# Kernel tuning notes

Hardware: AMD Instinct MI355X
Metric: run time of the kernel (lower is better)

## Reference

```python
import jax, jax.numpy as jnp
import numpy as np

N, E = 50000, 800000
IN_DIM, HID, OUT = 128, 64, 64
NEG_SLOPE = 0.2  # PyG GATConv default leaky_relu slope


def glorot(key, shape):
    fan_in, fan_out = shape[0], shape[-1]
    lim = jnp.sqrt(6.0 / (fan_in + fan_out))
    return jax.random.uniform(key, shape, minval=-lim, maxval=lim, dtype=jnp.float32)


def setup_inputs() -> dict:
    key = jax.random.key(0)
    ks = jax.random.split(key, 10)
    x = jax.random.normal(ks[0], (N, IN_DIM), dtype=jnp.float32)
    edge_index = jax.random.randint(ks[1], (2, E), 0, N, dtype=jnp.int64)
    # GATConv layer 1: heads=2, concat=False
    W1 = glorot(ks[2], (IN_DIM, 2 * HID))
    att_src1 = glorot(ks[3], (1, 2, HID))[0]   # [2, HID]
    att_dst1 = glorot(ks[4], (1, 2, HID))[0]
    b1 = jnp.zeros((HID,), jnp.float32)
    # GATConv layer 2: heads=1, concat=False
    W2 = glorot(ks[5], (HID, OUT))
    att_src2 = glorot(ks[6], (1, 1, OUT))[0]   # [1, OUT]
    att_dst2 = glorot(ks[7], (1, 1, OUT))[0]
    b2 = jnp.zeros((OUT,), jnp.float32)
    return {"x": x, "edge_index": edge_index, "W1": W1, "att_src1": att_src1,
            "att_dst1": att_dst1, "b1": b1, "W2": W2, "att_src2": att_src2,
            "att_dst2": att_dst2, "b2": b2}


def gat_conv(x, src, dst, W, att_src, att_dst, bias, heads, out_ch):
    n = x.shape[0]
    h = (x @ W).reshape(n, heads, out_ch)              # [N,H,C]
    a_src = jnp.einsum('nhc,hc->nh', h, att_src)       # [N,H]
    a_dst = jnp.einsum('nhc,hc->nh', h, att_dst)
    e = jax.nn.leaky_relu(a_src[src] + a_dst[dst], NEG_SLOPE)  # [E,H]
    # softmax over incoming edges per destination node (stable)
    e_max = jax.ops.segment_max(e, dst, num_segments=n)
    ex = jnp.exp(e - e_max[dst])
    denom = jax.ops.segment_sum(ex, dst, num_segments=n)
    alpha = ex / (denom[dst] + 1e-16)                  # [E,H]
    msg = h[src] * alpha[:, :, None]                   # [E,H,C]
    out = jax.ops.segment_sum(msg, dst, num_segments=n)
    return out.mean(axis=1) + bias                     # concat=False -> head mean


def reference(x, edge_index, W1, att_src1, att_dst1, b1, W2, att_src2, att_dst2, b2):
    n = x.shape[0]
    loop = jnp.arange(n, dtype=edge_index.dtype)
    src = jnp.concatenate([edge_index[0], loop])       # PyG add_self_loops
    dst = jnp.concatenate([edge_index[1], loop])
    x1 = gat_conv(x, src, dst, W1, att_src1, att_dst1, b1, 2, HID)
    x1 = jax.nn.elu(x1)
    # eval mode: dropedge and dropout are identity
    out = gat_conv(x1, src, dst, W2, att_src2, att_dst2, b2, 1, OUT)
    return out
```

## Files before the change

### kernel.cpp

```cpp
#include <hip/hip_runtime.h>
#include <math.h>

#define IN_DIM 128
#define HID 64
#define CAP 64
#define NEG_SLOPE 0.2f

__device__ __forceinline__ float wmax(float v){
  #pragma unroll
  for (int o = 32; o > 0; o >>= 1) v = fmaxf(v, __shfl_xor(v, o));
  return v;
}
__device__ __forceinline__ float wsum(float v){
  #pragma unroll
  for (int o = 32; o > 0; o >>= 1) v += __shfl_xor(v, o);
  return v;
}

__device__ __forceinline__ unsigned short f2bf(float f){
  union { float f; unsigned u; } v; v.f = f;
  unsigned r = v.u + 0x7fffu + ((v.u >> 16) & 1u);
  return (unsigned short)(r >> 16);
}
__device__ __forceinline__ float bl(unsigned u){
  union { unsigned u; float f; } v; v.u = u << 16; return v.f;
}
__device__ __forceinline__ float bh(unsigned u){
  union { unsigned u; float f; } v; v.u = u & 0xffff0000u; return v.f;
}

__global__ void build_buckets(const int* __restrict__ ei, int E,
                              int* __restrict__ cnt, int* __restrict__ bucket){
  int e = blockIdx.x * 256 + threadIdx.x;
  if (e >= E) return;
  int s = ei[e];
  int d = ei[E + e];
  int p = atomicAdd(&cnt[d], 1);
  if (p < CAP) bucket[d * CAP + p] = s;
}

template<int K, int NC, int HEADS>
__global__ __launch_bounds__(256) void gemm_mfma(const float* __restrict__ X,
    const float* __restrict__ Wm, const float* __restrict__ asrc,
    const float* __restrict__ adst, unsigned short* __restrict__ Hb,
    float* __restrict__ aa, int n_rows)
{
  typedef __attribute__((ext_vector_type(8))) short bf16x8;
  typedef __attribute__((ext_vector_type(4))) float f32x4;
  constexpr int KP = K + 8;
  constexpr int CP = NC + 4;
  constexpr unsigned SM1 = (unsigned)(64 + NC) * KP * 2;
  constexpr unsigned SM2 = (unsigned)64 * CP * 4;
  __shared__ char smem[SM1 > SM2 ? SM1 : SM2];
  unsigned short* xa = (unsigned short*)smem;
  unsigned short* wt = xa + 64 * KP;
  int tid = threadIdx.x;
  int n0 = blockIdx.x * 64;

  for (int idx = tid; idx < 64 * (K / 4); idx += 256){
    int n  = idx / (K / 4);
    int k4 = idx % (K / 4);
    float4 v = make_float4(0.f, 0.f, 0.f, 0.f);
    if (n0 + n < n_rows) v = *(const float4*)&X[(size_t)(n0 + n) * K + k4 * 4];
    ushort4 pk; pk.x = f2bf(v.x); pk.y = f2bf(v.y); pk.z = f2bf(v.z); pk.w = f2bf(v.w);
    *(ushort4*)&xa[n * KP + k4 * 4] = pk;
  }
  for (int idx = tid; idx < (K / 2) * (NC / 4); idx += 256){
    int kp = idx / (NC / 4);
    int n4 = idx % (NC / 4);
    float4 wa = *(const float4*)&Wm[(size_t)(2 * kp) * NC + n4 * 4];
    float4 wb = *(const float4*)&Wm[(size_t)(2 * kp + 1) * NC + n4 * 4];
    const float* pa = &wa.x; const float* pb = &wb.x;
    #pragma unroll
    for (int u = 0; u < 4; u++){
      unsigned val = (unsigned)f2bf(pa[u]) | ((unsigned)f2bf(pb[u]) << 16);
      *(unsigned*)&wt[(n4 * 4 + u) * KP + 2 * kp] = val;
    }
  }
  __syncthreads();

  int lane = tid & 63, w = tid >> 6;
  int m = lane & 15, q = lane >> 4;
  constexpr int NF = NC / 64;
  int n_base = w * (NC / 4);
  f32x4 acc[4][NF];
  #pragma unroll
  for (int i = 0; i < 4; i++)
    #pragma unroll
    for (int j = 0; j < NF; j++)
      #pragma unroll
      for (int r = 0; r < 4; r++) acc[i][j][r] = 0.f;

  #pragma unroll
  for (int ks = 0; ks < K / 32; ks++){
    bf16x8 af[4], bg[NF];
    #pragma unroll
    for (int m4 = 0; m4 < 4; m4++)
      af[m4] = *(const bf16x8*)&xa[(m4 * 16 + m) * KP + ks * 32 + q * 8];
    #pragma unroll
    for (int nf = 0; nf < NF; nf++)
      bg[nf] = *(const bf16x8*)&wt[(n_base + nf * 16 + m) * KP + ks * 32 + q * 8];
    #pragma unroll
    for (int m4 = 0; m4 < 4; m4++)
      #pragma unroll
      for (int nf = 0; nf < NF; nf++)
        acc[m4][nf] = __builtin_amdgcn_mfma_f32_16x16x32_bf16(af[m4], bg[nf], acc[m4][nf], 0, 0, 0);
  }
  __syncthreads();
  float* C = (float*)smem;
  #pragma unroll
  for (int m4 = 0; m4 < 4; m4++)
    #pragma unroll
    for (int nf = 0; nf < NF; nf++)
      #pragma unroll
      for (int r = 0; r < 4; r++)
        C[(m4 * 16 + q * 4 + r) * CP + n_base + nf * 16 + m] = acc[m4][nf][r];
  __syncthreads();

  constexpr int CH = NC / 4;
  int row = tid >> 2;
  int c0 = (tid & 3) * CH;
  int n = n0 + row;
  int head = (HEADS == 2) ? (c0 >> 6) : 0;
  float s_p = 0.f, d_p = 0.f;
  unsigned short hb[CH];
  #pragma unroll
  for (int c = 0; c < CH; c += 4){
    f32x4 v = *(const f32x4*)&C[row * CP + c0 + c];
    #pragma unroll
    for (int u = 0; u < 4; u++){
      int ch = (c0 + c + u) & 63;
      s_p += v[u] * asrc[head * 64 + ch];
      d_p += v[u] * adst[head * 64 + ch];
      hb[c + u] = f2bf(v[u]);
    }
  }
  if (n < n_rows){
    #pragma unroll
    for (int c = 0; c < CH; c += 8){
      uint4 pk;
      pk.x = (unsigned)hb[c]     | ((unsigned)hb[c + 1] << 16);
      pk.y = (unsigned)hb[c + 2] | ((unsigned)hb[c + 3] << 16);
      pk.z = (unsigned)hb[c + 4] | ((unsigned)hb[c + 5] << 16);
      pk.w = (unsigned)hb[c + 6] | ((unsigned)hb[c + 7] << 16);
      *(uint4*)&Hb[(size_t)n * NC + c0 + c] = pk;
    }
  }
  s_p += __shfl_xor(s_p, 1);
  d_p += __shfl_xor(d_p, 1);
  if (HEADS == 2){
    if ((tid & 1) == 0 && n < n_rows){
      aa[(size_t)n * 4 + head]     = s_p;
      aa[(size_t)n * 4 + 2 + head] = d_p;
    }
  } else {
    s_p += __shfl_xor(s_p, 2);
    d_p += __shfl_xor(d_p, 2);
    if ((tid & 3) == 0 && n < n_rows){
      aa[(size_t)n * 2]     = s_p;
      aa[(size_t)n * 2 + 1] = d_p;
    }
  }
}

__global__ void agg_layer1(const int* __restrict__ cnt, const int* __restrict__ bucket,
                           const float* __restrict__ aa, const unsigned short* __restrict__ h1b,
                           const float* __restrict__ b1, float* __restrict__ x1, int n_nodes){
  int d = (blockIdx.x * blockDim.x + threadIdx.x) >> 6;
  int lane = threadIdx.x & 63;
  if (d >= n_nodes) return;
  int deg = cnt[d]; deg = deg < CAP ? deg : CAP;
  float2 adv = *(const float2*)&aa[d * 4 + 2];
  int s = -1;
  if (lane < deg) s = bucket[d * CAP + lane];
  else if (lane == deg) s = d;
  float e0 = -INFINITY, e1 = -INFINITY;
  if (s >= 0){
    float2 asv = *(const float2*)&aa[s * 4];
    float t0 = asv.x + adv.x;
    float t1 = asv.y + adv.y;
    e0 = t0 >= 0.f ? t0 : NEG_SLOPE * t0;
    e1 = t1 >= 0.f ? t1 : NEG_SLOPE * t1;
  }
  float m0 = wmax(e0), m1 = wmax(e1);
  float p0 = (s >= 0) ? __expf(e0 - m0) : 0.f;
  float p1 = (s >= 0) ? __expf(e1 - m1) : 0.f;
  float al0 = p0 / (wsum(p0) + 1e-16f);
  float al1 = p1 / (wsum(p1) + 1e-16f);
  int ne = deg + 1;
  int g = lane >> 4, c = lane & 15;
  float acc[8] = {0.f,0.f,0.f,0.f,0.f,0.f,0.f,0.f};
  #pragma unroll 4
  for (int j0 = 0; j0 < ne; j0 += 4){
    int j = j0 + g;
    int jj = j < ne ? j : 0;
    int sj = __shfl(s, jj);
    float a0 = __shfl(al0, jj);
    float a1 = __shfl(al1, jj);
    if (j >= ne){ a0 = 0.f; a1 = 0.f; }
    uint4 v = ((const uint4*)(h1b + (size_t)sj * 128))[c];
    float a = (c < 8) ? a0 : a1;
    acc[0] += a * bl(v.x); acc[1] += a * bh(v.x);
    acc[2] += a * bl(v.y); acc[3] += a * bh(v.y);
    acc[4] += a * bl(v.z); acc[5] += a * bh(v.z);
    acc[6] += a * bl(v.w); acc[7] += a * bh(v.w);
  }
  #pragma unroll
  for (int i = 0; i < 8; i++){
    acc[i] += __shfl_xor(acc[i], 16);
    acc[i] += __shfl_xor(acc[i], 32);
  }
  float outv[8];
  #pragma unroll
  for (int i = 0; i < 8; i++){
    float o = __shfl_xor(acc[i], 8);
    outv[i] = 0.5f * (acc[i] + o);
  }
  if (g == 0 && c < 8){
    float r[8];
    #pragma unroll
    for (int i = 0; i < 8; i++){
      float v = outv[i] + b1[c * 8 + i];
      r[i] = v > 0.f ? v : expm1f(v);
    }
    float* p = &x1[(size_t)d * 64 + c * 8];
    *(float4*)p       = make_float4(r[0], r[1], r[2], r[3]);
    *(float4*)(p + 4) = make_float4(r[4], r[5], r[6], r[7]);
  }
}

__global__ void agg_layer2(const int* __restrict__ cnt, const int* __restrict__ bucket,
                           const float* __restrict__ aa, const unsigned short* __restrict__ h2b,
                           const float* __restrict__ b2, float* __restrict__ out, int n_nodes){
  int d = (blockIdx.x * blockDim.x + threadIdx.x) >> 6;
  int lane = threadIdx.x & 63;
  if (d >= n_nodes) return;
  int deg = cnt[d]; deg = deg < CAP ? deg : CAP;
  float ad = aa[d * 2 + 1];
  int s = -1;
  if (lane < deg) s = bucket[d * CAP + lane];
  else if (lane == deg) s = d;
  float e = -INFINITY;
  if (s >= 0){
    float t = aa[s * 2 + 0] + ad;
    e = t >= 0.f ? t : NEG_SLOPE * t;
  }
  float m = wmax(e);
  float p = (s >= 0) ? __expf(e - m) : 0.f;
  float al = p / (wsum(p) + 1e-16f);
  int ne = deg + 1;
  int g = lane >> 3, c = lane & 7;
  float acc[8] = {0.f,0.f,0.f,0.f,0.f,0.f,0.f,0.f};
  #pragma unroll 4
  for (int j0 = 0; j0 < ne; j0 += 8){
    int j = j0 + g;
    int jj = j < ne ? j : 0;
    int sj = __shfl(s, jj);
    float a = __shfl(al, jj);
    if (j >= ne) a = 0.f;
    uint4 v = ((const uint4*)(h2b + (size_t)sj * 64))[c];
    acc[0] += a * bl(v.x); acc[1] += a * bh(v.x);
    acc[2] += a * bl(v.y); acc[3] += a * bh(v.y);
    acc[4] += a * bl(v.z); acc[5] += a * bh(v.z);
    acc[6] += a * bl(v.w); acc[7] += a * bh(v.w);
  }
  #pragma unroll
  for (int i = 0; i < 8; i++){
    acc[i] += __shfl_xor(acc[i], 8);
    acc[i] += __shfl_xor(acc[i], 16);
    acc[i] += __shfl_xor(acc[i], 32);
  }
  if (lane < 8){
    float r[8];
    #pragma unroll
    for (int i = 0; i < 8; i++) r[i] = acc[i] + b2[lane * 8 + i];
    float* q = &out[(size_t)d * 64 + lane * 8];
    *(float4*)q       = make_float4(r[0], r[1], r[2], r[3]);
    *(float4*)(q + 4) = make_float4(r[4], r[5], r[6], r[7]);
  }
}

extern "C" void kernel_launch(void* const* d_in, const int* in_sizes, int n_in,
                              void* d_out, int out_size, void* d_ws, size_t ws_size,
                              hipStream_t stream){
  const float* x     = (const float*)d_in[0];
  const int*   ei    = (const int*)d_in[1];
  const float* W1    = (const float*)d_in[2];
  const float* asrc1 = (const float*)d_in[3];
  const float* adst1 = (const float*)d_in[4];
  const float* b1    = (const float*)d_in[5];
  const float* W2    = (const float*)d_in[6];
  const float* asrc2 = (const float*)d_in[7];
  const float* adst2 = (const float*)d_in[8];
  const float* b2    = (const float*)d_in[9];
  float* out = (float*)d_out;
  int N = in_sizes[0] / IN_DIM;
  int E = in_sizes[1] / 2;

  char* p = (char*)d_ws;
  unsigned short* h1b = (unsigned short*)p;  p += (size_t)N * 128 * 2;
  unsigned short* h2b = (unsigned short*)p;  p += (size_t)N * 64 * 2;
  float* x1  = (float*)p;                    p += (size_t)N * 64 * 4;
  float* aa1 = (float*)p;                    p += (size_t)N * 4 * 4;
  float* aa2 = (float*)p;                    p += (size_t)N * 2 * 4;
  int* cnt    = (int*)p;                     p += (size_t)N * 4;
  int* bucket = (int*)p;

  hipMemsetAsync(cnt, 0, N * sizeof(int), stream);
  build_buckets<<<(E + 255) / 256, 256, 0, stream>>>(ei, E, cnt, bucket);
  gemm_mfma<128, 128, 2><<<(N + 63) / 64, 256, 0, stream>>>(
      x, W1, asrc1, adst1, h1b, aa1, N);
  agg_layer1<<<(N + 3) / 4, 256, 0, stream>>>(cnt, bucket, aa1, h1b, b1, x1, N);
  gemm_mfma<64, 64, 1><<<(N + 63) / 64, 256, 0, stream>>>(
      x1, W2, asrc2, adst2, h2b, aa2, N);
  agg_layer2<<<(N + 3) / 4, 256, 0, stream>>>(cnt, bucket, aa2, h2b, b2, out, N);
}
```

Before: 253.1 us.

## Pre-transpose weights to bf16, enlarge GEMM tiles, pack FMAs in aggregation

Adds a small kernel that converts and transposes W1/W2 to bf16 once, so each GEMM block copies ready-made weight rows instead of converting fp32 per block. The GEMM now processes 128-row tiles with 512 threads, each warp owning one 16-column fragment. The aggregation loops use packed two-wide float FMAs and skip the gather load for padded slots instead of loading a dummy row. The cost is an extra kernel launch and a different per-warp MFMA mapping.

After: 251.2 us. About the same (-0.8%).

```diff
diff --git a/kernel.cpp b/kernel.cpp
--- a/kernel.cpp
+++ b/kernel.cpp
@@ -6,6 +6,10 @@
 #define CAP 64
 #define NEG_SLOPE 0.2f
 
+typedef __attribute__((ext_vector_type(8))) short bf16x8;
+typedef __attribute__((ext_vector_type(4))) float f32x4;
+typedef __attribute__((ext_vector_type(2))) float v2f;
+
 __device__ __forceinline__ float wmax(float v){
   #pragma unroll
   for (int o = 32; o > 0; o >>= 1) v = fmaxf(v, __shfl_xor(v, o));
@@ -27,6 +31,23 @@
 }
 __device__ __forceinline__ float bh(unsigned u){
   union { unsigned u; float f; } v; v.u = u & 0xffff0000u; return v.f;
+}
+__device__ __forceinline__ v2f up2(unsigned u){
+  v2f r; r[0] = bl(u); r[1] = bh(u); return r;
+}
+
+__global__ void convert_w(const float* __restrict__ W1, const float* __restrict__ W2,
+                          unsigned short* __restrict__ W1t, unsigned short* __restrict__ W2t){
+  int tid = blockIdx.x * 256 + threadIdx.x;
+  if (tid < 128 * 128){
+    int n = tid >> 7, k = tid & 127;
+    W1t[n * 128 + k] = f2bf(W1[k * 128 + n]);
+  }
+  int t2 = tid - 128 * 128;
+  if (t2 >= 0 && t2 < 64 * 64){
+    int n = t2 >> 6, k = t2 & 63;
+    W2t[n * 64 + k] = f2bf(W2[k * 64 + n]);
+  }
 }
 
 __global__ void build_buckets(const int* __restrict__ ei, int E,
@@ -40,81 +61,66 @@
 }
 
 template<int K, int NC, int HEADS>
-__global__ __launch_bounds__(256) void gemm_mfma(const float* __restrict__ X,
-    const float* __restrict__ Wm, const float* __restrict__ asrc,
+__global__ __launch_bounds__(512) void gemm_mfma(const float* __restrict__ X,
+    const unsigned short* __restrict__ Wt, const float* __restrict__ asrc,
     const float* __restrict__ adst, unsigned short* __restrict__ Hb,
     float* __restrict__ aa, int n_rows)
 {
-  typedef __attribute__((ext_vector_type(8))) short bf16x8;
-  typedef __attribute__((ext_vector_type(4))) float f32x4;
+  constexpr int MT = 128;
   constexpr int KP = K + 8;
   constexpr int CP = NC + 4;
-  constexpr unsigned SM1 = (unsigned)(64 + NC) * KP * 2;
-  constexpr unsigned SM2 = (unsigned)64 * CP * 4;
+  constexpr int MF = MT / 16;
+  constexpr int NFt = NC / 16;
+  constexpr int WPN = 8 / NFt;
+  constexpr int MFW = MF / WPN;
+  constexpr unsigned SM1 = (unsigned)(MT + NC) * KP * 2;
+  constexpr unsigned SM2 = (unsigned)MT * CP * 4;
   __shared__ char smem[SM1 > SM2 ? SM1 : SM2];
   unsigned short* xa = (unsigned short*)smem;
-  unsigned short* wt = xa + 64 * KP;
+  unsigned short* wl = xa + MT * KP;
   int tid = threadIdx.x;
-  int n0 = blockIdx.x * 64;
-
-  for (int idx = tid; idx < 64 * (K / 4); idx += 256){
-    int n  = idx / (K / 4);
-    int k4 = idx % (K / 4);
+  int n0 = blockIdx.x * MT;
+
+  for (int idx = tid; idx < MT * (K / 4); idx += 512){
+    int n = idx / (K / 4), k4 = idx % (K / 4);
     float4 v = make_float4(0.f, 0.f, 0.f, 0.f);
     if (n0 + n < n_rows) v = *(const float4*)&X[(size_t)(n0 + n) * K + k4 * 4];
     ushort4 pk; pk.x = f2bf(v.x); pk.y = f2bf(v.y); pk.z = f2bf(v.z); pk.w = f2bf(v.w);
     *(ushort4*)&xa[n * KP + k4 * 4] = pk;
   }
-  for (int idx = tid; idx < (K / 2) * (NC / 4); idx += 256){
-    int kp = idx / (NC / 4);
-    int n4 = idx % (NC / 4);
-    float4 wa = *(const float4*)&Wm[(size_t)(2 * kp) * NC + n4 * 4];
-    float4 wb = *(const float4*)&Wm[(size_t)(2 * kp + 1) * NC + n4 * 4];
-    const float* pa = &wa.x; const float* pb = &wb.x;
-    #pragma unroll
-    for (int u = 0; u < 4; u++){
-      unsigned val = (unsigned)f2bf(pa[u]) | ((unsigned)f2bf(pb[u]) << 16);
-      *(unsigned*)&wt[(n4 * 4 + u) * KP + 2 * kp] = val;
-    }
+  for (int idx = tid; idx < NC * (K / 8); idx += 512){
+    int n = idx / (K / 8), k8 = idx % (K / 8);
+    uint4 v = *(const uint4*)&Wt[(size_t)n * K + k8 * 8];
+    *(uint4*)&wl[n * KP + k8 * 8] = v;
   }
   __syncthreads();
 
   int lane = tid & 63, w = tid >> 6;
   int m = lane & 15, q = lane >> 4;
-  constexpr int NF = NC / 64;
-  int n_base = w * (NC / 4);
-  f32x4 acc[4][NF];
-  #pragma unroll
-  for (int i = 0; i < 4; i++)
-    #pragma unroll
-    for (int j = 0; j < NF; j++)
-      #pragma unroll
-      for (int r = 0; r < 4; r++) acc[i][j][r] = 0.f;
+  int nf = w % NFt;
+  int mseg = w / NFt;
+  f32x4 acc[MFW];
+  #pragma unroll
+  for (int i = 0; i < MFW; i++)
+    #pragma unroll
+    for (int r = 0; r < 4; r++) acc[i][r] = 0.f;
 
   #pragma unroll
   for (int ks = 0; ks < K / 32; ks++){
-    bf16x8 af[4], bg[NF];
-    #pragma unroll
-    for (int m4 = 0; m4 < 4; m4++)
-      af[m4] = *(const bf16x8*)&xa[(m4 * 16 + m) * KP + ks * 32 + q * 8];
-    #pragma unroll
-    for (int nf = 0; nf < NF; nf++)
-      bg[nf] = *(const bf16x8*)&wt[(n_base + nf * 16 + m) * KP + ks * 32 + q * 8];
-    #pragma unroll
-    for (int m4 = 0; m4 < 4; m4++)
-      #pragma unroll
-      for (int nf = 0; nf < NF; nf++)
-        acc[m4][nf] = __builtin_amdgcn_mfma_f32_16x16x32_bf16(af[m4], bg[nf], acc[m4][nf], 0, 0, 0);
+    bf16x8 bg = *(const bf16x8*)&wl[(nf * 16 + m) * KP + ks * 32 + q * 8];
+    #pragma unroll
+    for (int i = 0; i < MFW; i++){
+      bf16x8 af = *(const bf16x8*)&xa[((mseg * MFW + i) * 16 + m) * KP + ks * 32 + q * 8];
+      acc[i] = __builtin_amdgcn_mfma_f32_16x16x32_bf16(af, bg, acc[i], 0, 0, 0);
+    }
   }
   __syncthreads();
   float* C = (float*)smem;
   #pragma unroll
-  for (int m4 = 0; m4 < 4; m4++)
-    #pragma unroll
-    for (int nf = 0; nf < NF; nf++)
-      #pragma unroll
-      for (int r = 0; r < 4; r++)
-        C[(m4 * 16 + q * 4 + r) * CP + n_base + nf * 16 + m] = acc[m4][nf][r];
+  for (int i = 0; i < MFW; i++)
+    #pragma unroll
+    for (int r = 0; r < 4; r++)
+      C[((mseg * MFW + i) * 16 + q * 4 + r) * CP + nf * 16 + m] = acc[i][r];
   __syncthreads();
 
   constexpr int CH = NC / 4;
@@ -189,32 +195,35 @@
   float al1 = p1 / (wsum(p1) + 1e-16f);
   int ne = deg + 1;
   int g = lane >> 4, c = lane & 15;
-  float acc[8] = {0.f,0.f,0.f,0.f,0.f,0.f,0.f,0.f};
-  #pragma unroll 4
+  v2f acc[4] = {{0.f,0.f},{0.f,0.f},{0.f,0.f},{0.f,0.f}};
+  #pragma unroll 2
   for (int j0 = 0; j0 < ne; j0 += 4){
     int j = j0 + g;
-    int jj = j < ne ? j : 0;
-    int sj = __shfl(s, jj);
-    float a0 = __shfl(al0, jj);
-    float a1 = __shfl(al1, jj);
-    if (j >= ne){ a0 = 0.f; a1 = 0.f; }
-    uint4 v = ((const uint4*)(h1b + (size_t)sj * 128))[c];
-    float a = (c < 8) ? a0 : a1;
-    acc[0] += a * bl(v.x); acc[1] += a * bh(v.x);
-    acc[2] += a * bl(v.y); acc[3] += a * bh(v.y);
-    acc[4] += a * bl(v.z); acc[5] += a * bh(v.z);
-    acc[6] += a * bl(v.w); acc[7] += a * bh(v.w);
-  }
+    int sj = __shfl(s, j);
+    float a0 = __shfl(al0, j);
+    float a1 = __shfl(al1, j);
+    if (j < ne){
+      uint4 v = ((const uint4*)(h1b + (size_t)sj * 128))[c];
+      float a = (c < 8) ? a0 : a1;
+      v2f av = {a, a};
+      acc[0] = av * up2(v.x) + acc[0];
+      acc[1] = av * up2(v.y) + acc[1];
+      acc[2] = av * up2(v.z) + acc[2];
+      acc[3] = av * up2(v.w) + acc[3];
+    }
+  }
+  float accf[8] = {acc[0][0], acc[0][1], acc[1][0], acc[1][1],
+                   acc[2][0], acc[2][1], acc[3][0], acc[3][1]};
   #pragma unroll
   for (int i = 0; i < 8; i++){
-    acc[i] += __shfl_xor(acc[i], 16);
-    acc[i] += __shfl_xor(acc[i], 32);
+    accf[i] += __shfl_xor(accf[i], 16);
+    accf[i] += __shfl_xor(accf[i], 32);
   }
   float outv[8];
   #pragma unroll
   for (int i = 0; i < 8; i++){
-    float o = __shfl_xor(acc[i], 8);
-    outv[i] = 0.5f * (acc[i] + o);
+    float o = __shfl_xor(accf[i], 8);
+    outv[i] = 0.5f * (accf[i] + o);
   }
   if (g == 0 && c < 8){
     float r[8];
@@ -250,30 +259,33 @@
   float al = p / (wsum(p) + 1e-16f);
   int ne = deg + 1;
   int g = lane >> 3, c = lane & 7;
-  float acc[8] = {0.f,0.f,0.f,0.f,0.f,0.f,0.f,0.f};
-  #pragma unroll 4
+  v2f acc[4] = {{0.f,0.f},{0.f,0.f},{0.f,0.f},{0.f,0.f}};
+  #pragma unroll 2
   for (int j0 = 0; j0 < ne; j0 += 8){
     int j = j0 + g;
-    int jj = j < ne ? j : 0;
-    int sj = __shfl(s, jj);
-    float a = __shfl(al, jj);
-    if (j >= ne) a = 0.f;
-    uint4 v = ((const uint4*)(h2b + (size_t)sj * 64))[c];
-    acc[0] += a * bl(v.x); acc[1] += a * bh(v.x);
-    acc[2] += a * bl(v.y); acc[3] += a * bh(v.y);
-    acc[4] += a * bl(v.z); acc[5] += a * bh(v.z);
-    acc[6] += a * bl(v.w); acc[7] += a * bh(v.w);
-  }
+    int sj = __shfl(s, j);
+    float a = __shfl(al, j);
+    if (j < ne){
+      uint4 v = ((const uint4*)(h2b + (size_t)sj * 64))[c];
+      v2f av = {a, a};
+      acc[0] = av * up2(v.x) + acc[0];
+      acc[1] = av * up2(v.y) + acc[1];
+      acc[2] = av * up2(v.z) + acc[2];
+      acc[3] = av * up2(v.w) + acc[3];
+    }
+  }
+  float accf[8] = {acc[0][0], acc[0][1], acc[1][0], acc[1][1],
+                   acc[2][0], acc[2][1], acc[3][0], acc[3][1]};
   #pragma unroll
   for (int i = 0; i < 8; i++){
-    acc[i] += __shfl_xor(acc[i], 8);
-    acc[i] += __shfl_xor(acc[i], 16);
-    acc[i] += __shfl_xor(acc[i], 32);
+    accf[i] += __shfl_xor(accf[i], 8);
+    accf[i] += __shfl_xor(accf[i], 16);
+    accf[i] += __shfl_xor(accf[i], 32);
   }
   if (lane < 8){
     float r[8];
     #pragma unroll
-    for (int i = 0; i < 8; i++) r[i] = acc[i] + b2[lane * 8 + i];
+    for (int i = 0; i < 8; i++) r[i] = accf[i] + b2[lane * 8 + i];
     float* q = &out[(size_t)d * 64 + lane * 8];
     *(float4*)q       = make_float4(r[0], r[1], r[2], r[3]);
     *(float4*)(q + 4) = make_float4(r[4], r[5], r[6], r[7]);
@@ -304,14 +316,17 @@
   float* aa1 = (float*)p;                    p += (size_t)N * 4 * 4;
   float* aa2 = (float*)p;                    p += (size_t)N * 2 * 4;
   int* cnt    = (int*)p;                     p += (size_t)N * 4;
-  int* bucket = (int*)p;
+  int* bucket = (int*)p;                     p += (size_t)N * CAP * 4;
+  unsigned short* W1t = (unsigned short*)p;  p += 128 * 128 * 2;
+  unsigned short* W2t = (unsigned short*)p;
 
   hipMemsetAsync(cnt, 0, N * sizeof(int), stream);
+  convert_w<<<(128 * 128 + 64 * 64 + 255) / 256, 256, 0, stream>>>(W1, W2, W1t, W2t);
   build_buckets<<<(E + 255) / 256, 256, 0, stream>>>(ei, E, cnt, bucket);
-  gemm_mfma<128, 128, 2><<<(N + 63) / 64, 256, 0, stream>>>(
-      x, W1, asrc1, adst1, h1b, aa1, N);
+  gemm_mfma<128, 128, 2><<<(N + 127) / 128, 512, 0, stream>>>(
+      x, W1t, asrc1, adst1, h1b, aa1, N);
   agg_layer1<<<(N + 3) / 4, 256, 0, stream>>>(cnt, bucket, aa1, h1b, b1, x1, N);
-  gemm_mfma<64, 64, 1><<<(N + 63) / 64, 256, 0, stream>>>(
-      x1, W2, asrc2, adst2, h2b, aa2, N);
+  gemm_mfma<64, 64, 1><<<(N + 127) / 128, 512, 0, stream>>>(
+      x1, W2t, asrc2, adst2, h2b, aa2, N);
   agg_layer2<<<(N + 3) / 4, 256, 0, stream>>>(cnt, bucket, aa2, h2b, b2, out, N);
 }
```
